# Kernel optimization log

Measured on AMD Instinct MI355X. Metric: run time of the kernel, lower is better.

## Reference

```python
import jax, jax.numpy as jnp
import numpy as np

N = 50000      # node_size
D = 256        # node_F == rel_F (ent_F)
R = 1000       # rel_size
E = 300000     # triple_size == n_edges
DEPTH = 2
KSEL = E // 2  # rows rewritten by W_orth transform
NPROXY = 128


def l2n(x):
    # tf.nn.l2_normalize with eps=1e-12
    return x * jax.lax.rsqrt(jnp.maximum(jnp.sum(x * x, axis=-1, keepdims=True), 1e-12))


def setup_inputs() -> dict:
    key = jax.random.key(0)
    ks = jax.random.split(key, 12)
    features = jax.random.normal(ks[0], (N, D), jnp.float32)
    rel_emb = jax.random.normal(ks[1], (R, D), jnp.float32)
    p = jax.random.normal(ks[2], (N, 1), jnp.float32)            # dynamic_node_kernel
    w_keys = jax.random.normal(ks[3], (DEPTH, D, D), jnp.float32) / np.float32(np.sqrt(D))
    attn_kernels = jax.random.normal(ks[4], (DEPTH, D, 1), jnp.float32) * 0.1
    proxy = jax.random.normal(ks[5], (NPROXY, D * (DEPTH + 1)), jnp.float32) * 0.05
    gate_kernel = jax.random.normal(ks[6], (D * (DEPTH + 1), D * (DEPTH + 1)), jnp.float32) / np.float32(np.sqrt(D * (DEPTH + 1)))
    adj_row = jnp.sort(jax.random.randint(ks[7], (E,), 0, N))    # destination (segment) ids, sorted
    adj_col = jax.random.randint(ks[8], (E,), 0, N)              # neighbor ids
    rel_ids = jax.random.randint(ks[9], (E,), 0, R)              # relation id per triple/edge
    rel_vals = jax.random.uniform(ks[10], (E,), jnp.float32)     # sparse_val per triple
    new_indices = jax.random.randint(ks[11], (KSEL,), 0, E)      # rows updated by w_key
    return dict(features=features, rel_emb=rel_emb, p=p, w_keys=w_keys,
                attn_kernels=attn_kernels, proxy=proxy, gate_kernel=gate_kernel,
                rel_vals=rel_vals, adj_row=adj_row, adj_col=adj_col,
                rel_ids=rel_ids, new_indices=new_indices)


def reference(features, rel_emb, p, w_keys, attn_kernels, proxy, gate_kernel,
              rel_vals, adj_row, adj_col, rel_ids, new_indices):
    tanh_p = jnp.tanh(p)                                   # [N,1]
    feats = features * tanh_p                              # use_p scaling (activation=None -> identity)
    outputs = [feats]
    for l in range(DEPTH):
        # sparse (triple,rel) x rel_emb : one relation per triple -> gather + scale
        rels_sum = rel_vals[:, None] * rel_emb[rel_ids]    # [E,D]
        rels_sum = l2n(rels_sum)
        # W_orth: transform a subset of rows by w_key, scatter back
        src = rels_sum[new_indices] @ w_keys[l]            # [KSEL,D]
        rels_sum = rels_sum.at[new_indices].set(src)
        neighs = feats[adj_col]                            # [E,D] gather
        rels_sum = rels_sum * tanh_p[adj_col]              # use_p on neighbors
        # Householder-style reflection of neighbor features
        neighs = neighs - 2.0 * jnp.sum(neighs * rels_sum, axis=1, keepdims=True) * rels_sum
        # per-edge attention logits, softmax over incoming edges of each row node
        att = (rels_sum @ attn_kernels[l])[:, 0]           # [E]
        m = jax.ops.segment_max(att, adj_row, num_segments=N)      # [N]
        att = jnp.exp(att - m[adj_row])
        s = jax.ops.segment_sum(att, adj_row, num_segments=N)      # [N]
        att = att / s[adj_row]
        # weighted scatter-aggregate
        feats = jax.ops.segment_sum(neighs * att[:, None], adj_row, num_segments=N)  # [N,D]
        feats = feats * tanh_p
        outputs.append(feats)
    out = jnp.concatenate(outputs, axis=-1)                # [N, D*(DEPTH+1)]
    proxy_att = jax.nn.softmax(l2n(out) @ l2n(proxy).T, axis=-1)   # [N,128]
    proxy_feature = out - proxy_att @ proxy
    gate = jax.nn.sigmoid(proxy_feature @ gate_kernel)
    out = gate * out + (1.0 - gate) * proxy_feature
    return (out, p)
```

## Files before the change

kernel.cpp:

```cpp
#include <hip/hip_runtime.h>
#include <math.h>

#define D 256
#define DCAT 768
#define NPX 128
#define QSTR 896
#define CSTR 136

typedef __attribute__((ext_vector_type(8))) short bf16x8;
typedef __attribute__((ext_vector_type(4))) float f32x4;

__device__ __forceinline__ short cvt_bf16(float f){
  union { float f; unsigned u; } v; v.f = f;
  unsigned r = v.u + 0x7FFF + ((v.u >> 16) & 1);
  return (short)(r >> 16);
}
__device__ __forceinline__ float bf2f(short s){
  union { float f; unsigned u; } v; v.u = ((unsigned)(unsigned short)s) << 16;
  return v.f;
}

__device__ __forceinline__ float waveSum(float v){
#pragma unroll
  for(int o=32;o>=1;o>>=1) v += __shfl_xor(v,o,64);
  return v;
}
__device__ __forceinline__ float waveMax(float v){
#pragma unroll
  for(int o=32;o>=1;o>>=1) v = fmaxf(v,__shfl_xor(v,o,64));
  return v;
}

__global__ void k_prep(const float* __restrict__ p, float* __restrict__ tp,
                       const int* __restrict__ adj_row, int* __restrict__ rs,
                       const int* __restrict__ idx, unsigned char* __restrict__ flag,
                       float* __restrict__ pout, int n, int e, int ksel){
  int i = blockIdx.x*blockDim.x+threadIdx.x;
  if(i<n){ float pv = p[i]; tp[i]=tanhf(pv); pout[i]=pv; }
  if(i<=n){
    int lo=0, hi=e;
    while(lo<hi){ int mid=(lo+hi)>>1; if(adj_row[mid]<i) lo=mid+1; else hi=mid; }
    rs[i]=lo;
  }
  if(i<ksel) flag[idx[i]] = 1;
}

__global__ void k_relprep(const float* __restrict__ rel_emb, const float* __restrict__ attn,
                          float* __restrict__ ss_rel, float* __restrict__ att_n,
                          short* __restrict__ reb, int R_){
  __shared__ float sm[4];
  int r = blockIdx.x; int d = threadIdx.x;
  float v = rel_emb[(size_t)r*D+d];
  reb[(size_t)r*D+d] = cvt_bf16(v);
  int lane=threadIdx.x&63, wid=threadIdx.x>>6;
  float s = waveSum(v*v);
  if(lane==0) sm[wid]=s;
  __syncthreads();
  if(threadIdx.x==0) ss_rel[r]=sm[0]+sm[1]+sm[2]+sm[3];
  __syncthreads();
  for(int l=0;l<2;l++){
    float dd = waveSum(v*attn[l*D+d]);
    if(lane==0) sm[wid]=dd;
    __syncthreads();
    if(threadIdx.x==0) att_n[(size_t)l*R_+r]=sm[0]+sm[1]+sm[2]+sm[3];
    __syncthreads();
  }
}

__global__ void k_relW(const float* __restrict__ rel_emb, const float* __restrict__ W,
                       const float* __restrict__ ak, short* __restrict__ rwb,
                       float* __restrict__ att_t, int R_){
  __shared__ float sm[4];
  int r=blockIdx.x, d=threadIdx.x;
  const float* row = rel_emb + (size_t)r*D;
  float acc=0.f;
#pragma unroll 4
  for(int k=0;k<D;k++) acc = fmaf(row[k], W[(size_t)k*D+d], acc);
  rwb[(size_t)r*D+d]=cvt_bf16(acc);
  int lane=threadIdx.x&63, wid=threadIdx.x>>6;
  float dd = waveSum(acc*ak[d]);
  if(lane==0) sm[wid]=dd;
  __syncthreads();
  if(threadIdx.x==0) att_t[r]=sm[0]+sm[1]+sm[2]+sm[3];
}

__global__ void k_init0(const float* __restrict__ features, const float* __restrict__ tp,
                        short* __restrict__ Q, float* __restrict__ ssn, int n){
  __shared__ float sm[4];
  int row = blockIdx.x, d = threadIdx.x;
  float v = features[(size_t)row*D + d] * tp[row];
  Q[(size_t)row*QSTR + d] = cvt_bf16(v);
  int lane=d&63, wid=d>>6;
  float s = waveSum(v*v);
  if(lane==0) sm[wid]=s;
  __syncthreads();
  if(d==0) ssn[row] = sm[0]+sm[1]+sm[2]+sm[3];
}

__global__ void k_agg(const int* __restrict__ rs, const int* __restrict__ adj_col,
                      const int* __restrict__ rel_ids, const float* __restrict__ rel_vals,
                      const unsigned char* __restrict__ flag, const float* __restrict__ tp,
                      const float* __restrict__ ss_rel, const float* __restrict__ att_n,
                      const float* __restrict__ att_t, const short* __restrict__ reb,
                      const short* __restrict__ rwb, short* __restrict__ Q,
                      float* __restrict__ ssn, int n, int layer){
  int wid = threadIdx.x>>6, lane = threadIdx.x&63;
  int node = blockIdx.x*4 + wid;
  if(node>=n) return;
  int s = rs[node], e = rs[node+1];
  float accq[16];
#pragma unroll
  for(int k=0;k<16;k++) accq[k]=0.f;
  if(e > s){
    float mx = -INFINITY;
    for(int i=s+lane;i<e;i+=64){
      int rid = rel_ids[i]; float rv = rel_vals[i];
      float a = 0.f;
      if(rv>0.f){
        float t = tp[adj_col[i]];
        float sc = rv*rsqrtf(fmaxf(rv*rv*ss_rel[rid],1e-12f));
        a = t*sc*(flag[i]? att_t[rid] : att_n[rid]);
      }
      mx = fmaxf(mx,a);
    }
    mx = waveMax(mx);
    float se = 0.f;
    for(int i=s+lane;i<e;i+=64){
      int rid = rel_ids[i]; float rv = rel_vals[i];
      float a = 0.f;
      if(rv>0.f){
        float t = tp[adj_col[i]];
        float sc = rv*rsqrtf(fmaxf(rv*rv*ss_rel[rid],1e-12f));
        a = t*sc*(flag[i]? att_t[rid] : att_n[rid]);
      }
      se += __expf(a-mx);
    }
    se = waveSum(se);
    float inv = 1.f/se;
    int qid = lane>>4, ql = lane&15;
    for(int i0=s; i0<e; i0+=4){
      int j = i0 + qid;
      float w=0.f, coef=0.f;
      float nbv[16], rbv[16];
#pragma unroll
      for(int k=0;k<16;k++){ nbv[k]=0.f; rbv[k]=0.f; }
      if(j < e){
        int rid = rel_ids[j]; float rv = rel_vals[j]; int col = adj_col[j];
        const short* np = Q + (size_t)col*QSTR + layer*D + ql*16;
        bf16x8 n0 = *(const bf16x8*)np;
        bf16x8 n1 = *(const bf16x8*)(np+8);
#pragma unroll
        for(int k=0;k<8;k++){ nbv[k]=bf2f(n0[k]); nbv[k+8]=bf2f(n1[k]); }
        if(rv>0.f){
          float t = tp[col];
          float sc = rv*rsqrtf(fmaxf(rv*rv*ss_rel[rid],1e-12f));
          bool f = flag[j];
          const short* rp = (f? rwb : reb) + (size_t)rid*D + ql*16;
          bf16x8 r0 = *(const bf16x8*)rp;
          bf16x8 r1 = *(const bf16x8*)(rp+8);
#pragma unroll
          for(int k=0;k<8;k++){ rbv[k]=bf2f(r0[k]); rbv[k+8]=bf2f(r1[k]); }
          float dp = 0.f;
#pragma unroll
          for(int k=0;k<16;k++) dp += nbv[k]*rbv[k];
#pragma unroll
          for(int o=1;o<16;o<<=1) dp += __shfl_xor(dp,o,64);
          float a = t*sc*(f? att_t[rid] : att_n[rid]);
          w = __expf(a-mx)*inv;
          coef = 2.f*t*t*sc*sc*dp;
        } else {
          w = __expf(-mx)*inv;
        }
      }
#pragma unroll
      for(int k=0;k<16;k++) accq[k] += w*(nbv[k] - coef*rbv[k]);
    }
  }
#pragma unroll
  for(int k=0;k<16;k++){
    float v = accq[k];
    v += __shfl_xor(v,16,64);
    v += __shfl_xor(v,32,64);
    accq[k] = v;
  }
  if(lane < 16){
    float t0 = tp[node];
    bf16x8 o0, o1;
    float pss = 0.f;
#pragma unroll
    for(int k=0;k<8;k++){
      o0[k]=cvt_bf16(accq[k]*t0); o1[k]=cvt_bf16(accq[k+8]*t0);
      pss += accq[k]*accq[k] + accq[k+8]*accq[k+8];
    }
    short* op = Q + (size_t)node*QSTR + (layer+1)*D + lane*16;
    *(bf16x8*)op = o0;
    *(bf16x8*)(op+8) = o1;
#pragma unroll
    for(int o=1;o<16;o<<=1) pss += __shfl_xor(pss,o,64);
    if(lane==0) ssn[node] += pss * t0 * t0;
  }
}

__global__ void k_proxynorm(const float* __restrict__ proxy, short* __restrict__ pn){
  __shared__ float sm[4];
  int j = blockIdx.x;
  float ssum=0.f;
  for(int d=threadIdx.x; d<DCAT; d+=256){ float v=proxy[(size_t)j*DCAT+d]; ssum+=v*v; }
  int lane=threadIdx.x&63, wid=threadIdx.x>>6;
  ssum = waveSum(ssum);
  if(lane==0) sm[wid]=ssum;
  __syncthreads();
  float scale = rsqrtf(fmaxf(sm[0]+sm[1]+sm[2]+sm[3],1e-12f));
  for(int d=threadIdx.x; d<DCAT; d+=256)
    pn[(size_t)j*DCAT + d] = cvt_bf16(proxy[(size_t)j*DCAT+d]*scale);
}

__global__ void k_cast(const float* __restrict__ in, short* __restrict__ out, long total){
  long i = (long)blockIdx.x*blockDim.x+threadIdx.x;
  if(i<total) out[i]=cvt_bf16(in[i]);
}

__global__ void k_tcast(const float* __restrict__ in, short* __restrict__ out,
                        int R, int C, int ldo, int coff, float sign){
  __shared__ float tile[32][33];
  int bx = blockIdx.x*32, by = blockIdx.y*32;
  for(int i=threadIdx.y;i<32;i+=8){
    int rr = by+i, cc = bx+threadIdx.x;
    if(rr<R && cc<C) tile[i][threadIdx.x] = in[(size_t)rr*C + cc];
  }
  __syncthreads();
  for(int i=threadIdx.y;i<32;i+=8){
    int cc = bx+i, rr = by+threadIdx.x;
    if(cc<C && rr<R) out[(size_t)cc*ldo + coff + rr] = cvt_bf16(sign*tile[threadIdx.x][i]);
  }
}

template<int LDA_, int LDB_, int NTOT, int KC>
__global__ __launch_bounds__(256,2) void k_gemm(
    const short* __restrict__ A, const short* __restrict__ Bt,
    float* __restrict__ outF, int M)
{
  __shared__ short smem[3][2][128*32];
  const int tid = threadIdx.x;
  const int lane = tid & 63, w = tid >> 6;
  const int wm = w >> 1, wn = w & 1;
  const int bn = blockIdx.x * 128, bm = blockIdx.y * 128;

  const short* Ag = A  + (size_t)bm * LDA_;
  const short* Bg = Bt + (size_t)bn * LDB_;

  auto stage = [&](int buf, int k0){
#pragma unroll
    for(int c=0;c<2;++c){
      int u = c*256 + tid;
      int row = u >> 2;
      int cb = ((u & 3) ^ ((u >> 3) & 3)) * 8;
      __builtin_amdgcn_global_load_lds(
        (const __attribute__((address_space(1))) unsigned int*)(Ag + (size_t)row*LDA_ + k0 + cb),
        (__attribute__((address_space(3))) unsigned int*)&smem[buf][0][u*8], 16, 0, 0);
      __builtin_amdgcn_global_load_lds(
        (const __attribute__((address_space(1))) unsigned int*)(Bg + (size_t)row*LDB_ + k0 + cb),
        (__attribute__((address_space(3))) unsigned int*)&smem[buf][1][u*8], 16, 0, 0);
    }
  };

  f32x4 acc[4][4] = {};
  const int lr = lane & 15, kg = lane >> 4;
  const int ksw = (kg ^ ((lr >> 1) & 3)) * 8;
  constexpr int NT = KC / 32;

  stage(0, 0);
  stage(1, 32);
  for(int t=0; t<NT; ++t){
    if(t+1 < NT) asm volatile("s_waitcnt vmcnt(4)" ::: "memory");
    else         asm volatile("s_waitcnt vmcnt(0)" ::: "memory");
    __builtin_amdgcn_s_barrier();
    __builtin_amdgcn_sched_barrier(0);
    const short* Al = &smem[t%3][0][0];
    const short* Bl = &smem[t%3][1][0];
    bf16x8 af[4], bfr[4];
#pragma unroll
    for(int i=0;i<4;++i) af[i] = *(const bf16x8*)(Al + (wm*64 + i*16 + lr)*32 + ksw);
#pragma unroll
    for(int j=0;j<4;++j) bfr[j] = *(const bf16x8*)(Bl + (wn*64 + j*16 + lr)*32 + ksw);
    if(t+2 < NT) stage((t+2)%3, (t+2)*32);
    __builtin_amdgcn_s_setprio(1);
#pragma unroll
    for(int i=0;i<4;++i)
#pragma unroll
      for(int j=0;j<4;++j)
        acc[i][j] = __builtin_amdgcn_mfma_f32_16x16x32_bf16(af[i], bfr[j], acc[i][j], 0, 0, 0);
    __builtin_amdgcn_s_setprio(0);
  }

  const int row0 = bm + wm*64 + (lane>>4)*4;
  const int col0 = bn + wn*64 + lr;
#pragma unroll
  for(int i=0;i<4;++i)
#pragma unroll
    for(int j=0;j<4;++j)
#pragma unroll
      for(int r=0;r<4;++r){
        int row = row0 + i*16 + r;
        if(row < M) outF[(size_t)row*NTOT + col0 + j*16] = acc[i][j][r];
      }
}

__global__ __launch_bounds__(256,2) void k_pr(
    short* __restrict__ Q, const short* __restrict__ pn,
    const float* __restrict__ ssn, int M)
{
  __shared__ short smem[3][2][128*32];
  const int tid = threadIdx.x, lane = tid & 63, w = tid >> 6;
  const int wm = w >> 1, wn = w & 1;
  int nwg = gridDim.y;
  int orig = blockIdx.y;
  int q = nwg>>3, rm = nwg&7, xcd = orig&7, lid = orig>>3;
  int wg = (xcd<rm ? xcd*(q+1) : rm*(q+1)+(xcd-rm)*q) + lid;
  const int bm = wg*128;

  const short* Ag = Q + (size_t)bm * QSTR;
  const short* Bg = pn;

  auto stage = [&](int buf, int k0){
#pragma unroll
    for(int c=0;c<2;++c){
      int u = c*256 + tid;
      int row = u >> 2;
      int cb = ((u & 3) ^ ((u >> 3) & 3)) * 8;
      __builtin_amdgcn_global_load_lds(
        (const __attribute__((address_space(1))) unsigned int*)(Ag + (size_t)row*QSTR + k0 + cb),
        (__attribute__((address_space(3))) unsigned int*)&smem[buf][0][u*8], 16, 0, 0);
      __builtin_amdgcn_global_load_lds(
        (const __attribute__((address_space(1))) unsigned int*)(Bg + (size_t)row*DCAT + k0 + cb),
        (__attribute__((address_space(3))) unsigned int*)&smem[buf][1][u*8], 16, 0, 0);
    }
  };

  f32x4 acc[4][4] = {};
  const int lr = lane & 15, kg = lane >> 4;
  const int ksw = (kg ^ ((lr >> 1) & 3)) * 8;
  constexpr int NT = DCAT / 32;

  stage(0, 0);
  stage(1, 32);
  for(int t=0; t<NT; ++t){
    if(t+1 < NT) asm volatile("s_waitcnt vmcnt(4)" ::: "memory");
    else         asm volatile("s_waitcnt vmcnt(0)" ::: "memory");
    __builtin_amdgcn_s_barrier();
    __builtin_amdgcn_sched_barrier(0);
    const short* Al = &smem[t%3][0][0];
    const short* Bl = &smem[t%3][1][0];
    bf16x8 af[4], bfr[4];
#pragma unroll
    for(int i=0;i<4;++i) af[i] = *(const bf16x8*)(Al + (wm*64 + i*16 + lr)*32 + ksw);
#pragma unroll
    for(int j=0;j<4;++j) bfr[j] = *(const bf16x8*)(Bl + (wn*64 + j*16 + lr)*32 + ksw);
    if(t+2 < NT) stage((t+2)%3, (t+2)*32);
    __builtin_amdgcn_s_setprio(1);
#pragma unroll
    for(int i=0;i<4;++i)
#pragma unroll
      for(int j=0;j<4;++j)
        acc[i][j] = __builtin_amdgcn_mfma_f32_16x16x32_bf16(af[i], bfr[j], acc[i][j], 0, 0, 0);
    __builtin_amdgcn_s_setprio(0);
  }

  __syncthreads();
  short* lg = (short*)smem;
  const int row0l = wm*64 + kg*4;
  const int col0l = wn*64 + lr;
#pragma unroll
  for(int i=0;i<4;++i){
#pragma unroll
    for(int j=0;j<4;++j){
#pragma unroll
      for(int r=0;r<4;++r){
        int rl = row0l + i*16 + r;
        int rg = bm + rl;
        float s = (rg < M) ? rsqrtf(fmaxf(ssn[rg],1e-12f)) : 0.f;
        lg[rl*132 + col0l + j*16] = cvt_bf16(acc[i][j][r] * s);
      }
    }
  }
  __syncthreads();
  for(int k2=0;k2<32;++k2){
    int rl = w*32 + k2;
    float a = bf2f(lg[rl*132 + lane]);
    float b = bf2f(lg[rl*132 + 64 + lane]);
    float m = waveMax(fmaxf(a,b));
    float ea = __expf(a-m), eb = __expf(b-m);
    float sm_ = waveSum(ea+eb);
    float inv = 1.f/sm_;
    size_t rg = (size_t)(bm + rl);
    Q[rg*QSTR + DCAT + lane]      = cvt_bf16(ea*inv);
    Q[rg*QSTR + DCAT + 64 + lane] = cvt_bf16(eb*inv);
  }
}

__global__ __launch_bounds__(256,2) void k_go(
    short* __restrict__ Q, const short* __restrict__ BG,
    const short* __restrict__ Bt2, float* __restrict__ outF, int M)
{
  __shared__ short smem[3][2][128*32];
  const int tid = threadIdx.x, lane = tid & 63, w = tid >> 6;
  const int wm = w >> 1, wn = w & 1;
  const int gx = gridDim.x;
  int nwg = gx*gridDim.y;
  int orig = blockIdx.y*gx + blockIdx.x;
  int q = nwg>>3, rm = nwg&7, xcd = orig&7, lid = orig>>3;
  int wg = (xcd<rm ? xcd*(q+1) : rm*(q+1)+(xcd-rm)*q) + lid;
  const int bn = (wg%gx)*128, bm = (wg/gx)*128;
  const int lr = lane & 15, kg = lane >> 4;

  const short* Ag = Q  + (size_t)bm * QSTR;
  const short* Bg = BG + (size_t)bn * QSTR;

  auto stage = [&](int buf, int k0){
#pragma unroll
    for(int c=0;c<2;++c){
      int u = c*256 + tid;
      int row = u >> 2;
      int cb = ((u & 3) ^ ((u >> 3) & 3)) * 8;
      __builtin_amdgcn_global_load_lds(
        (const __attribute__((address_space(1))) unsigned int*)(Ag + (size_t)row*QSTR + k0 + cb),
        (__attribute__((address_space(3))) unsigned int*)&smem[buf][0][u*8], 16, 0, 0);
      __builtin_amdgcn_global_load_lds(
        (const __attribute__((address_space(1))) unsigned int*)(Bg + (size_t)row*QSTR + k0 + cb),
        (__attribute__((address_space(3))) unsigned int*)&smem[buf][1][u*8], 16, 0, 0);
    }
  };

  stage(0, 0);
  stage(1, 32);

  f32x4 acc[4][4] = {};
#pragma unroll
  for(int ks=0; ks<4; ++ks){
    bf16x8 af[4], bb[4];
#pragma unroll
    for(int i=0;i<4;++i)
      af[i] = *(const bf16x8*)(Q + (size_t)(bm + wm*64 + i*16 + lr)*QSTR + DCAT + ks*32 + kg*8);
#pragma unroll
    for(int j=0;j<4;++j)
      bb[j] = *(const bf16x8*)(Bt2 + (size_t)(bn + wn*64 + j*16 + lr)*NPX + ks*32 + kg*8);
#pragma unroll
    for(int i=0;i<4;++i)
#pragma unroll
      for(int j=0;j<4;++j)
        acc[i][j] = __builtin_amdgcn_mfma_f32_16x16x32_bf16(af[i], bb[j], acc[i][j], 0, 0, 0);
  }
  short4 pvb[4][4];
#pragma unroll
  for(int i=0;i<4;++i)
#pragma unroll
    for(int j=0;j<4;++j){
      pvb[i][j].x = cvt_bf16(acc[i][j][0]);
      pvb[i][j].y = cvt_bf16(acc[i][j][1]);
      pvb[i][j].z = cvt_bf16(acc[i][j][2]);
      pvb[i][j].w = cvt_bf16(acc[i][j][3]);
      acc[i][j] = (f32x4){0.f,0.f,0.f,0.f};
    }

  const int ksw = (kg ^ ((lr >> 1) & 3)) * 8;
  constexpr int NT = QSTR / 32;
  for(int t=0; t<NT; ++t){
    if(t+1 < NT) asm volatile("s_waitcnt vmcnt(4)" ::: "memory");
    else         asm volatile("s_waitcnt vmcnt(0)" ::: "memory");
    __builtin_amdgcn_s_barrier();
    __builtin_amdgcn_sched_barrier(0);
    const short* Al = &smem[t%3][0][0];
    const short* Bl = &smem[t%3][1][0];
    bf16x8 af[4], bfr[4];
#pragma unroll
    for(int i=0;i<4;++i) af[i] = *(const bf16x8*)(Al + (wm*64 + i*16 + lr)*32 + ksw);
#pragma unroll
    for(int j=0;j<4;++j) bfr[j] = *(const bf16x8*)(Bl + (wn*64 + j*16 + lr)*32 + ksw);
    if(t+2 < NT) stage((t+2)%3, (t+2)*32);
    __builtin_amdgcn_s_setprio(1);
#pragma unroll
    for(int i=0;i<4;++i)
#pragma unroll
      for(int j=0;j<4;++j)
        acc[i][j] = __builtin_amdgcn_mfma_f32_16x16x32_bf16(af[i], bfr[j], acc[i][j], 0, 0, 0);
    __builtin_amdgcn_s_setprio(0);
  }

  __syncthreads();
  short* cst = (short*)smem;
  const int row0l = wm*64 + kg*4;
  const int col0l = wn*64 + lr;
#pragma unroll
  for(int i=0;i<4;++i){
#pragma unroll
    for(int j=0;j<4;++j){
      float pv4[4] = { bf2f(pvb[i][j].x), bf2f(pvb[i][j].y), bf2f(pvb[i][j].z), bf2f(pvb[i][j].w) };
#pragma unroll
      for(int r2=0;r2<4;++r2){
        float g = 1.f/(1.f+__expf(-acc[i][j][r2]));
        cst[(row0l + i*16 + r2)*CSTR + col0l + j*16] = cvt_bf16((1.f-g)*pv4[r2]);
      }
    }
  }
  __syncthreads();
  const int rl0 = tid>>4, c0 = (tid&15)*8;
#pragma unroll
  for(int rr=0; rr<8; ++rr){
    int rl = rl0 + rr*16;
    int rg = bm + rl;
    if(rg >= M) continue;
    bf16x8 c8  = *(const bf16x8*)(cst + rl*CSTR + c0);
    bf16x8 oc8 = *(const bf16x8*)(Q + (size_t)rg*QSTR + bn + c0);
    float ov[8];
#pragma unroll
    for(int k=0;k<8;k++) ov[k] = bf2f(oc8[k]) - bf2f(c8[k]);
    *(float4*)(outF + (size_t)rg*DCAT + bn + c0)     = make_float4(ov[0],ov[1],ov[2],ov[3]);
    *(float4*)(outF + (size_t)rg*DCAT + bn + c0 + 4) = make_float4(ov[4],ov[5],ov[6],ov[7]);
  }
}

extern "C" void kernel_launch(void* const* d_in, const int* in_sizes, int n_in,
                              void* d_out, int out_size, void* d_ws, size_t ws_size,
                              hipStream_t stream){
  const float* features = (const float*)d_in[0];
  const float* rel_emb  = (const float*)d_in[1];
  const float* p        = (const float*)d_in[2];
  const float* w_keys   = (const float*)d_in[3];
  const float* attn     = (const float*)d_in[4];
  const float* proxy    = (const float*)d_in[5];
  const float* gatek    = (const float*)d_in[6];
  const float* rel_vals = (const float*)d_in[7];
  const int* adj_row    = (const int*)d_in[8];
  const int* adj_col    = (const int*)d_in[9];
  const int* rel_ids    = (const int*)d_in[10];
  const int* new_idx    = (const int*)d_in[11];

  const int n    = in_sizes[2];
  const int r    = in_sizes[1]/D;
  const int e    = in_sizes[7];
  const int ksel = in_sizes[11];
  const size_t Mpad = ((size_t)n + 127) & ~(size_t)127;

  char* ws = (char*)d_ws;
  size_t off=0;
  auto alloc=[&](size_t bytes)->void*{ void* pp = ws+off; off=(off+bytes+255)&~(size_t)255; return pp; };
  float* tp      = (float*)alloc((size_t)n*4);
  int*   rs      = (int*)alloc((size_t)(n+1)*4);
  unsigned char* flag = (unsigned char*)alloc((size_t)e);
  float* ss_rel  = (float*)alloc((size_t)r*4);
  float* att_n   = (float*)alloc((size_t)2*r*4);
  float* att_t   = (float*)alloc((size_t)2*r*4);
  short* reb     = (short*)alloc((size_t)r*D*2);
  short* rwb     = (short*)alloc((size_t)2*r*D*2);
  short* pn      = (short*)alloc((size_t)NPX*DCAT*2);
  short* proxyb  = (short*)alloc((size_t)NPX*DCAT*2);
  short* Bt2     = (short*)alloc((size_t)DCAT*NPX*2);
  short* BG      = (short*)alloc((size_t)DCAT*QSTR*2);
  float* MxF     = (float*)alloc((size_t)NPX*DCAT*4);
  float* ssn     = (float*)alloc(Mpad*4);
  short* Q       = (short*)alloc(Mpad*QSTR*2);

  float* outF = (float*)d_out;
  float* pout = (float*)d_out + (size_t)n*DCAT;

  hipMemsetAsync(flag, 0, (size_t)e, stream);
  hipMemsetAsync(Q + (size_t)n*QSTR, 0, (Mpad-(size_t)n)*QSTR*2, stream);

  int prep_n = (ksel > n+1 ? ksel : n+1);
  k_prep<<<(prep_n+255)/256,256,0,stream>>>(p,tp,adj_row,rs,new_idx,flag,pout,n,e,ksel);
  k_relprep<<<r,256,0,stream>>>(rel_emb,attn,ss_rel,att_n,reb,r);
  for(int l=0;l<2;l++)
    k_relW<<<r,256,0,stream>>>(rel_emb, w_keys+(size_t)l*D*D, attn+(size_t)l*D,
                               rwb+(size_t)l*r*D, att_t+(size_t)l*r, r);
  k_proxynorm<<<NPX,256,0,stream>>>(proxy,pn);
  {
    long tpx = (long)NPX*DCAT;
    k_cast<<<(int)((tpx+255)/256),256,0,stream>>>(proxy, proxyb, tpx);
    dim3 tb(32,8);
    k_tcast<<<dim3(DCAT/32, DCAT/32), tb, 0, stream>>>(gatek, BG, DCAT, DCAT, QSTR, 0, 1.f);
    k_gemm<DCAT, QSTR, DCAT, DCAT><<<dim3(DCAT/128,1),256,0,stream>>>(proxyb, BG, MxF, NPX);
    k_tcast<<<dim3(DCAT/32, NPX/32), tb, 0, stream>>>(MxF, BG, NPX, DCAT, QSTR, DCAT, -1.f);
    k_tcast<<<dim3(DCAT/32, NPX/32), tb, 0, stream>>>(proxy, Bt2, NPX, DCAT, NPX, 0, 1.f);
  }
  k_init0<<<n,256,0,stream>>>(features,tp,Q,ssn,n);
  for(int l=0;l<2;l++)
    k_agg<<<(n+3)/4,256,0,stream>>>(rs,adj_col,rel_ids,rel_vals,flag,tp,ss_rel,
                                    att_n+(size_t)l*r, att_t+(size_t)l*r, reb,
                                    rwb+(size_t)l*r*D, Q, ssn, n, l);

  int mt = (int)(Mpad/128);
  k_pr<<<dim3(1, mt),256,0,stream>>>(Q, pn, ssn, n);
  k_go<<<dim3(DCAT/128, mt),256,0,stream>>>(Q, BG, Bt2, outF, n);
}
```

Measured before the change: 495.9 us.

## Enlarge k_go row tile to 256 with 512 threads and defer proxy GEMM

The gate GEMM kernel now uses 512-thread workgroups that compute 256-row by 128-column tiles. Each B tile staged in LDS is therefore reused by eight waves instead of four, which cuts B-side global traffic per output. The small proxy_att@proxy GEMM is moved from before the main K loop to after it, so its bf16 results no longer occupy registers during the pipelined loop. In exchange the launch has half as many workgroups, uses more LDS per block, and pads M to 256, which can lower occupancy and load balance.

After: 505.5 us. About the same (+1.9%).

```diff
diff --git a/kernel.cpp b/kernel.cpp
--- a/kernel.cpp
+++ b/kernel.cpp
@@ -398,20 +398,20 @@
   }
 }
 
-__global__ __launch_bounds__(256,2) void k_go(
+__global__ __launch_bounds__(512,2) void k_go(
     short* __restrict__ Q, const short* __restrict__ BG,
     const short* __restrict__ Bt2, float* __restrict__ outF, int M)
 {
-  __shared__ short smem[3][2][128*32];
+  __shared__ short smem[3][384*32];
   const int tid = threadIdx.x, lane = tid & 63, w = tid >> 6;
   const int wm = w >> 1, wn = w & 1;
+  const int lr = lane & 15, kg = lane >> 4;
   const int gx = gridDim.x;
   int nwg = gx*gridDim.y;
   int orig = blockIdx.y*gx + blockIdx.x;
   int q = nwg>>3, rm = nwg&7, xcd = orig&7, lid = orig>>3;
   int wg = (xcd<rm ? xcd*(q+1) : rm*(q+1)+(xcd-rm)*q) + lid;
-  const int bn = (wg%gx)*128, bm = (wg/gx)*128;
-  const int lr = lane & 15, kg = lane >> 4;
+  const int bn = (wg%gx)*128, bm = (wg/gx)*256;
 
   const short* Ag = Q  + (size_t)bm * QSTR;
   const short* Bg = BG + (size_t)bn * QSTR;
@@ -419,15 +419,20 @@
   auto stage = [&](int buf, int k0){
 #pragma unroll
     for(int c=0;c<2;++c){
-      int u = c*256 + tid;
+      int u = c*512 + tid;
       int row = u >> 2;
       int cb = ((u & 3) ^ ((u >> 3) & 3)) * 8;
       __builtin_amdgcn_global_load_lds(
         (const __attribute__((address_space(1))) unsigned int*)(Ag + (size_t)row*QSTR + k0 + cb),
-        (__attribute__((address_space(3))) unsigned int*)&smem[buf][0][u*8], 16, 0, 0);
+        (__attribute__((address_space(3))) unsigned int*)&smem[buf][u*8], 16, 0, 0);
+    }
+    {
+      int u = tid;
+      int row = u >> 2;
+      int cb = ((u & 3) ^ ((u >> 3) & 3)) * 8;
       __builtin_amdgcn_global_load_lds(
         (const __attribute__((address_space(1))) unsigned int*)(Bg + (size_t)row*QSTR + k0 + cb),
-        (__attribute__((address_space(3))) unsigned int*)&smem[buf][1][u*8], 16, 0, 0);
+        (__attribute__((address_space(3))) unsigned int*)&smem[buf][8192 + u*8], 16, 0, 0);
     }
   };
 
@@ -435,42 +440,15 @@
   stage(1, 32);
 
   f32x4 acc[4][4] = {};
-#pragma unroll
-  for(int ks=0; ks<4; ++ks){
-    bf16x8 af[4], bb[4];
-#pragma unroll
-    for(int i=0;i<4;++i)
-      af[i] = *(const bf16x8*)(Q + (size_t)(bm + wm*64 + i*16 + lr)*QSTR + DCAT + ks*32 + kg*8);
-#pragma unroll
-    for(int j=0;j<4;++j)
-      bb[j] = *(const bf16x8*)(Bt2 + (size_t)(bn + wn*64 + j*16 + lr)*NPX + ks*32 + kg*8);
-#pragma unroll
-    for(int i=0;i<4;++i)
-#pragma unroll
-      for(int j=0;j<4;++j)
-        acc[i][j] = __builtin_amdgcn_mfma_f32_16x16x32_bf16(af[i], bb[j], acc[i][j], 0, 0, 0);
-  }
-  short4 pvb[4][4];
-#pragma unroll
-  for(int i=0;i<4;++i)
-#pragma unroll
-    for(int j=0;j<4;++j){
-      pvb[i][j].x = cvt_bf16(acc[i][j][0]);
-      pvb[i][j].y = cvt_bf16(acc[i][j][1]);
-      pvb[i][j].z = cvt_bf16(acc[i][j][2]);
-      pvb[i][j].w = cvt_bf16(acc[i][j][3]);
-      acc[i][j] = (f32x4){0.f,0.f,0.f,0.f};
-    }
-
   const int ksw = (kg ^ ((lr >> 1) & 3)) * 8;
   constexpr int NT = QSTR / 32;
   for(int t=0; t<NT; ++t){
-    if(t+1 < NT) asm volatile("s_waitcnt vmcnt(4)" ::: "memory");
+    if(t+1 < NT) asm volatile("s_waitcnt vmcnt(3)" ::: "memory");
     else         asm volatile("s_waitcnt vmcnt(0)" ::: "memory");
     __builtin_amdgcn_s_barrier();
     __builtin_amdgcn_sched_barrier(0);
-    const short* Al = &smem[t%3][0][0];
-    const short* Bl = &smem[t%3][1][0];
+    const short* Al = &smem[t%3][0];
+    const short* Bl = &smem[t%3][0] + 8192;
     bf16x8 af[4], bfr[4];
 #pragma unroll
     for(int i=0;i<4;++i) af[i] = *(const bf16x8*)(Al + (wm*64 + i*16 + lr)*32 + ksw);
@@ -486,27 +464,51 @@
     __builtin_amdgcn_s_setprio(0);
   }
 
+  short4 omg[4][4];
+#pragma unroll
+  for(int i=0;i<4;++i)
+#pragma unroll
+    for(int j=0;j<4;++j){
+      omg[i][j].x = cvt_bf16(1.f - 1.f/(1.f+__expf(-acc[i][j][0])));
+      omg[i][j].y = cvt_bf16(1.f - 1.f/(1.f+__expf(-acc[i][j][1])));
+      omg[i][j].z = cvt_bf16(1.f - 1.f/(1.f+__expf(-acc[i][j][2])));
+      omg[i][j].w = cvt_bf16(1.f - 1.f/(1.f+__expf(-acc[i][j][3])));
+    }
+
+  f32x4 pv[4][4] = {};
+#pragma unroll
+  for(int ks=0; ks<4; ++ks){
+    bf16x8 af2[4];
+#pragma unroll
+    for(int i=0;i<4;++i)
+      af2[i] = *(const bf16x8*)(Q + (size_t)(bm + wm*64 + i*16 + lr)*QSTR + DCAT + ks*32 + kg*8);
+#pragma unroll
+    for(int j=0;j<4;++j){
+      bf16x8 bb = *(const bf16x8*)(Bt2 + (size_t)(bn + wn*64 + j*16 + lr)*NPX + ks*32 + kg*8);
+#pragma unroll
+      for(int i=0;i<4;++i)
+        pv[i][j] = __builtin_amdgcn_mfma_f32_16x16x32_bf16(af2[i], bb, pv[i][j], 0, 0, 0);
+    }
+  }
+
   __syncthreads();
   short* cst = (short*)smem;
   const int row0l = wm*64 + kg*4;
   const int col0l = wn*64 + lr;
 #pragma unroll
-  for(int i=0;i<4;++i){
+  for(int i=0;i<4;++i)
 #pragma unroll
     for(int j=0;j<4;++j){
-      float pv4[4] = { bf2f(pvb[i][j].x), bf2f(pvb[i][j].y), bf2f(pvb[i][j].z), bf2f(pvb[i][j].w) };
-#pragma unroll
-      for(int r2=0;r2<4;++r2){
-        float g = 1.f/(1.f+__expf(-acc[i][j][r2]));
-        cst[(row0l + i*16 + r2)*CSTR + col0l + j*16] = cvt_bf16((1.f-g)*pv4[r2]);
-      }
-    }
-  }
+      float o4[4] = { bf2f(omg[i][j].x), bf2f(omg[i][j].y), bf2f(omg[i][j].z), bf2f(omg[i][j].w) };
+#pragma unroll
+      for(int r2=0;r2<4;++r2)
+        cst[(row0l + i*16 + r2)*CSTR + col0l + j*16] = cvt_bf16(o4[r2]*pv[i][j][r2]);
+    }
   __syncthreads();
   const int rl0 = tid>>4, c0 = (tid&15)*8;
 #pragma unroll
   for(int rr=0; rr<8; ++rr){
-    int rl = rl0 + rr*16;
+    int rl = rl0 + rr*32;
     int rg = bm + rl;
     if(rg >= M) continue;
     bf16x8 c8  = *(const bf16x8*)(cst + rl*CSTR + c0);
@@ -539,7 +541,7 @@
   const int r    = in_sizes[1]/D;
   const int e    = in_sizes[7];
   const int ksel = in_sizes[11];
-  const size_t Mpad = ((size_t)n + 127) & ~(size_t)127;
+  const size_t Mpad = ((size_t)n + 255) & ~(size_t)255;
 
   char* ws = (char*)d_ws;
   size_t off=0;
@@ -588,7 +590,6 @@
                                     att_n+(size_t)l*r, att_t+(size_t)l*r, reb,
                                     rwb+(size_t)l*r*D, Q, ssn, n, l);
 
-  int mt = (int)(Mpad/128);
-  k_pr<<<dim3(1, mt),256,0,stream>>>(Q, pn, ssn, n);
-  k_go<<<dim3(DCAT/128, mt),256,0,stream>>>(Q, BG, Bt2, outF, n);
-}
+  k_pr<<<dim3(1, (int)(Mpad/128)),256,0,stream>>>(Q, pn, ssn, n);
+  k_go<<<dim3(DCAT/128, (int)(Mpad/256)),512,0,stream>>>(Q, BG, Bt2, outF, n);
+}
```

## Fuse setup kernels into one launch and prefetch edge metadata in aggregation

Applied to the files above, without the earlier changes.

Merges the relation prep, the two relation-weight projections, the proxy normalisation and cast, and the gate and proxy transposes into a single multi-role k_setup kernel. This cuts launch count and lets these independent jobs run concurrently. In k_agg, the first logit per lane is cached so the exp-sum pass recomputes one fewer logit. The next edge's column, relation id, value and flag are also loaded one iteration ahead to hide gather latency. The costs are higher register use in k_agg and block-role branching in k_setup.

New measurement: 444.3 us. 1.12x faster.

```diff
diff --git a/kernel.cpp b/kernel.cpp
--- a/kernel.cpp
+++ b/kernel.cpp
@@ -45,43 +45,94 @@
   if(i<ksel) flag[idx[i]] = 1;
 }
 
-__global__ void k_relprep(const float* __restrict__ rel_emb, const float* __restrict__ attn,
-                          float* __restrict__ ss_rel, float* __restrict__ att_n,
-                          short* __restrict__ reb, int R_){
+__global__ void k_setup(const float* __restrict__ rel_emb, const float* __restrict__ attn,
+                        const float* __restrict__ w_keys, const float* __restrict__ proxy,
+                        const float* __restrict__ gatek,
+                        float* __restrict__ ss_rel, float* __restrict__ att_n,
+                        float* __restrict__ att_t, short* __restrict__ reb,
+                        short* __restrict__ rwb, short* __restrict__ pn,
+                        short* __restrict__ proxyb, short* __restrict__ BG,
+                        short* __restrict__ Bt2, int R_){
+  __shared__ float tile[32][33];
   __shared__ float sm[4];
-  int r = blockIdx.x; int d = threadIdx.x;
-  float v = rel_emb[(size_t)r*D+d];
-  reb[(size_t)r*D+d] = cvt_bf16(v);
-  int lane=threadIdx.x&63, wid=threadIdx.x>>6;
-  float s = waveSum(v*v);
-  if(lane==0) sm[wid]=s;
+  const int b = blockIdx.x, tid = threadIdx.x;
+  const int lane = tid & 63, wv = tid >> 6;
+
+  if(b < R_){
+    int r = b, d = tid;
+    float v = rel_emb[(size_t)r*D+d];
+    reb[(size_t)r*D+d] = cvt_bf16(v);
+    float s = waveSum(v*v);
+    if(lane==0) sm[wv]=s;
+    __syncthreads();
+    if(tid==0) ss_rel[r]=sm[0]+sm[1]+sm[2]+sm[3];
+    __syncthreads();
+    for(int l=0;l<2;l++){
+      float dd = waveSum(v*attn[l*D+d]);
+      if(lane==0) sm[wv]=dd;
+      __syncthreads();
+      if(tid==0) att_n[(size_t)l*R_+r]=sm[0]+sm[1]+sm[2]+sm[3];
+      __syncthreads();
+    }
+  } else if(b < 3*R_){
+    int l = (b-R_) / R_, r = (b-R_) % R_, d = tid;
+    const float* W = w_keys + (size_t)l*D*D;
+    const float* ak = attn + (size_t)l*D;
+    const float* row = rel_emb + (size_t)r*D;
+    float acc=0.f;
+#pragma unroll 4
+    for(int k=0;k<D;k++) acc = fmaf(row[k], W[(size_t)k*D+d], acc);
+    rwb[(size_t)l*R_*D + (size_t)r*D + d]=cvt_bf16(acc);
+    float dd = waveSum(acc*ak[d]);
+    if(lane==0) sm[wv]=dd;
+    __syncthreads();
+    if(tid==0) att_t[(size_t)l*R_+r]=sm[0]+sm[1]+sm[2]+sm[3];
+  } else if(b < 3*R_+128){
+    int j = b - 3*R_;
+    float v0 = proxy[(size_t)j*DCAT + tid];
+    float v1 = proxy[(size_t)j*DCAT + 256 + tid];
+    float v2 = proxy[(size_t)j*DCAT + 512 + tid];
+    proxyb[(size_t)j*DCAT + tid]       = cvt_bf16(v0);
+    proxyb[(size_t)j*DCAT + 256 + tid] = cvt_bf16(v1);
+    proxyb[(size_t)j*DCAT + 512 + tid] = cvt_bf16(v2);
+    float ssum = waveSum(v0*v0 + v1*v1 + v2*v2);
+    if(lane==0) sm[wv]=ssum;
+    __syncthreads();
+    float scale = rsqrtf(fmaxf(sm[0]+sm[1]+sm[2]+sm[3],1e-12f));
+    pn[(size_t)j*DCAT + tid]       = cvt_bf16(v0*scale);
+    pn[(size_t)j*DCAT + 256 + tid] = cvt_bf16(v1*scale);
+    pn[(size_t)j*DCAT + 512 + tid] = cvt_bf16(v2*scale);
+  } else {
+    const float* in; short* out; int R, C, ldo, coff, t;
+    if(b < 3*R_+128+576){ t = b-(3*R_+128);     in=gatek; out=BG;  R=DCAT; C=DCAT; ldo=QSTR; coff=0; }
+    else                { t = b-(3*R_+128+576); in=proxy; out=Bt2; R=NPX;  C=DCAT; ldo=NPX;  coff=0; }
+    int bx = (t%24)*32, by = (t/24)*32;
+    int tx = tid & 31, ty = tid >> 5;
+    for(int i=ty;i<32;i+=8){
+      int rr = by+i, cc = bx+tx;
+      if(rr<R && cc<C) tile[i][tx] = in[(size_t)rr*C + cc];
+    }
+    __syncthreads();
+    for(int i=ty;i<32;i+=8){
+      int cc = bx+i, rr = by+tx;
+      if(cc<C && rr<R) out[(size_t)cc*ldo + coff + rr] = cvt_bf16(tile[tx][i]);
+    }
+  }
+}
+
+__global__ void k_tcast(const float* __restrict__ in, short* __restrict__ out,
+                        int R, int C, int ldo, int coff, float sign){
+  __shared__ float tile[32][33];
+  int bx = blockIdx.x*32, by = blockIdx.y*32;
+  for(int i=threadIdx.y;i<32;i+=8){
+    int rr = by+i, cc = bx+threadIdx.x;
+    if(rr<R && cc<C) tile[i][threadIdx.x] = in[(size_t)rr*C + cc];
+  }
   __syncthreads();
-  if(threadIdx.x==0) ss_rel[r]=sm[0]+sm[1]+sm[2]+sm[3];
-  __syncthreads();
-  for(int l=0;l<2;l++){
-    float dd = waveSum(v*attn[l*D+d]);
-    if(lane==0) sm[wid]=dd;
-    __syncthreads();
-    if(threadIdx.x==0) att_n[(size_t)l*R_+r]=sm[0]+sm[1]+sm[2]+sm[3];
-    __syncthreads();
-  }
-}
-
-__global__ void k_relW(const float* __restrict__ rel_emb, const float* __restrict__ W,
-                       const float* __restrict__ ak, short* __restrict__ rwb,
-                       float* __restrict__ att_t, int R_){
-  __shared__ float sm[4];
-  int r=blockIdx.x, d=threadIdx.x;
-  const float* row = rel_emb + (size_t)r*D;
-  float acc=0.f;
-#pragma unroll 4
-  for(int k=0;k<D;k++) acc = fmaf(row[k], W[(size_t)k*D+d], acc);
-  rwb[(size_t)r*D+d]=cvt_bf16(acc);
-  int lane=threadIdx.x&63, wid=threadIdx.x>>6;
-  float dd = waveSum(acc*ak[d]);
-  if(lane==0) sm[wid]=dd;
-  __syncthreads();
-  if(threadIdx.x==0) att_t[r]=sm[0]+sm[1]+sm[2]+sm[3];
+  for(int i=threadIdx.y;i<32;i+=8){
+    int cc = bx+i, rr = by+threadIdx.x;
+    if(cc<C && rr<R) out[(size_t)cc*ldo + coff + rr] = cvt_bf16(sign*tile[threadIdx.x][i]);
+  }
 }
 
 __global__ void k_init0(const float* __restrict__ features, const float* __restrict__ tp,
@@ -111,41 +162,50 @@
   float accq[16];
 #pragma unroll
   for(int k=0;k<16;k++) accq[k]=0.f;
+
+  auto logit = [&](int i)->float{
+    int rid = rel_ids[i]; float rv = rel_vals[i];
+    float a = 0.f;
+    if(rv>0.f){
+      float t = tp[adj_col[i]];
+      float sc = rv*rsqrtf(fmaxf(rv*rv*ss_rel[rid],1e-12f));
+      a = t*sc*(flag[i]? att_t[rid] : att_n[rid]);
+    }
+    return a;
+  };
+
   if(e > s){
-    float mx = -INFINITY;
-    for(int i=s+lane;i<e;i+=64){
-      int rid = rel_ids[i]; float rv = rel_vals[i];
-      float a = 0.f;
-      if(rv>0.f){
-        float t = tp[adj_col[i]];
-        float sc = rv*rsqrtf(fmaxf(rv*rv*ss_rel[rid],1e-12f));
-        a = t*sc*(flag[i]? att_t[rid] : att_n[rid]);
+    float aF = 0.f, mxl = -INFINITY;
+    {
+      int i = s + lane;
+      if(i < e){
+        aF = logit(i);
+        mxl = aF;
+        for(i += 64; i < e; i += 64) mxl = fmaxf(mxl, logit(i));
       }
-      mx = fmaxf(mx,a);
-    }
-    mx = waveMax(mx);
-    float se = 0.f;
-    for(int i=s+lane;i<e;i+=64){
-      int rid = rel_ids[i]; float rv = rel_vals[i];
-      float a = 0.f;
-      if(rv>0.f){
-        float t = tp[adj_col[i]];
-        float sc = rv*rsqrtf(fmaxf(rv*rv*ss_rel[rid],1e-12f));
-        a = t*sc*(flag[i]? att_t[rid] : att_n[rid]);
-      }
-      se += __expf(a-mx);
-    }
-    se = waveSum(se);
+    }
+    float mx = waveMax(mxl);
+    float sel = (s+lane < e) ? __expf(aF - mx) : 0.f;
+    for(int i = s+64+lane; i < e; i += 64) sel += __expf(logit(i) - mx);
+    float se = waveSum(sel);
     float inv = 1.f/se;
+
     int qid = lane>>4, ql = lane&15;
+    int j0 = s + qid;
+    bool valid = j0 < e;
+    int col=0, rid=0; float rv=0.f; bool fl=false;
+    if(valid){ col=adj_col[j0]; rid=rel_ids[j0]; rv=rel_vals[j0]; fl=flag[j0]; }
     for(int i0=s; i0<e; i0+=4){
-      int j = i0 + qid;
+      int jn = i0 + 4 + qid;
+      bool vn = jn < e;
+      int coln=0, ridn=0; float rvn=0.f; bool fln=false;
+      if(vn){ coln=adj_col[jn]; ridn=rel_ids[jn]; rvn=rel_vals[jn]; fln=flag[jn]; }
+
       float w=0.f, coef=0.f;
       float nbv[16], rbv[16];
 #pragma unroll
       for(int k=0;k<16;k++){ nbv[k]=0.f; rbv[k]=0.f; }
-      if(j < e){
-        int rid = rel_ids[j]; float rv = rel_vals[j]; int col = adj_col[j];
+      if(valid){
         const short* np = Q + (size_t)col*QSTR + layer*D + ql*16;
         bf16x8 n0 = *(const bf16x8*)np;
         bf16x8 n1 = *(const bf16x8*)(np+8);
@@ -154,8 +214,7 @@
         if(rv>0.f){
           float t = tp[col];
           float sc = rv*rsqrtf(fmaxf(rv*rv*ss_rel[rid],1e-12f));
-          bool f = flag[j];
-          const short* rp = (f? rwb : reb) + (size_t)rid*D + ql*16;
+          const short* rp = (fl? rwb : reb) + (size_t)rid*D + ql*16;
           bf16x8 r0 = *(const bf16x8*)rp;
           bf16x8 r1 = *(const bf16x8*)(rp+8);
 #pragma unroll
@@ -165,7 +224,7 @@
           for(int k=0;k<16;k++) dp += nbv[k]*rbv[k];
 #pragma unroll
           for(int o=1;o<16;o<<=1) dp += __shfl_xor(dp,o,64);
-          float a = t*sc*(f? att_t[rid] : att_n[rid]);
+          float a = t*sc*(fl? att_t[rid] : att_n[rid]);
           w = __expf(a-mx)*inv;
           coef = 2.f*t*t*sc*sc*dp;
         } else {
@@ -174,6 +233,8 @@
       }
 #pragma unroll
       for(int k=0;k<16;k++) accq[k] += w*(nbv[k] - coef*rbv[k]);
+
+      valid=vn; col=coln; rid=ridn; rv=rvn; fl=fln;
     }
   }
 #pragma unroll
@@ -198,40 +259,6 @@
 #pragma unroll
     for(int o=1;o<16;o<<=1) pss += __shfl_xor(pss,o,64);
     if(lane==0) ssn[node] += pss * t0 * t0;
-  }
-}
-
-__global__ void k_proxynorm(const float* __restrict__ proxy, short* __restrict__ pn){
-  __shared__ float sm[4];
-  int j = blockIdx.x;
-  float ssum=0.f;
-  for(int d=threadIdx.x; d<DCAT; d+=256){ float v=proxy[(size_t)j*DCAT+d]; ssum+=v*v; }
-  int lane=threadIdx.x&63, wid=threadIdx.x>>6;
-  ssum = waveSum(ssum);
-  if(lane==0) sm[wid]=ssum;
-  __syncthreads();
-  float scale = rsqrtf(fmaxf(sm[0]+sm[1]+sm[2]+sm[3],1e-12f));
-  for(int d=threadIdx.x; d<DCAT; d+=256)
-    pn[(size_t)j*DCAT + d] = cvt_bf16(proxy[(size_t)j*DCAT+d]*scale);
-}
-
-__global__ void k_cast(const float* __restrict__ in, short* __restrict__ out, long total){
-  long i = (long)blockIdx.x*blockDim.x+threadIdx.x;
-  if(i<total) out[i]=cvt_bf16(in[i]);
-}
-
-__global__ void k_tcast(const float* __restrict__ in, short* __restrict__ out,
-                        int R, int C, int ldo, int coff, float sign){
-  __shared__ float tile[32][33];
-  int bx = blockIdx.x*32, by = blockIdx.y*32;
-  for(int i=threadIdx.y;i<32;i+=8){
-    int rr = by+i, cc = bx+threadIdx.x;
-    if(rr<R && cc<C) tile[i][threadIdx.x] = in[(size_t)rr*C + cc];
-  }
-  __syncthreads();
-  for(int i=threadIdx.y;i<32;i+=8){
-    int cc = bx+i, rr = by+threadIdx.x;
-    if(cc<C && rr<R) out[(size_t)cc*ldo + coff + rr] = cvt_bf16(sign*tile[threadIdx.x][i]);
   }
 }
 
@@ -568,20 +595,15 @@
 
   int prep_n = (ksel > n+1 ? ksel : n+1);
   k_prep<<<(prep_n+255)/256,256,0,stream>>>(p,tp,adj_row,rs,new_idx,flag,pout,n,e,ksel);
-  k_relprep<<<r,256,0,stream>>>(rel_emb,attn,ss_rel,att_n,reb,r);
-  for(int l=0;l<2;l++)
-    k_relW<<<r,256,0,stream>>>(rel_emb, w_keys+(size_t)l*D*D, attn+(size_t)l*D,
-                               rwb+(size_t)l*r*D, att_t+(size_t)l*r, r);
-  k_proxynorm<<<NPX,256,0,stream>>>(proxy,pn);
   {
-    long tpx = (long)NPX*DCAT;
-    k_cast<<<(int)((tpx+255)/256),256,0,stream>>>(proxy, proxyb, tpx);
-    dim3 tb(32,8);
-    k_tcast<<<dim3(DCAT/32, DCAT/32), tb, 0, stream>>>(gatek, BG, DCAT, DCAT, QSTR, 0, 1.f);
-    k_gemm<DCAT, QSTR, DCAT, DCAT><<<dim3(DCAT/128,1),256,0,stream>>>(proxyb, BG, MxF, NPX);
-    k_tcast<<<dim3(DCAT/32, NPX/32), tb, 0, stream>>>(MxF, BG, NPX, DCAT, QSTR, DCAT, -1.f);
-    k_tcast<<<dim3(DCAT/32, NPX/32), tb, 0, stream>>>(proxy, Bt2, NPX, DCAT, NPX, 0, 1.f);
-  }
+    int nblocks = 3*r + 128 + 576 + 96;
+    k_setup<<<nblocks,256,0,stream>>>(rel_emb, attn, w_keys, proxy, gatek,
+                                      ss_rel, att_n, att_t, reb, rwb, pn, proxyb,
+                                      BG, Bt2, r);
+  }
+  k_gemm<DCAT, QSTR, DCAT, DCAT><<<dim3(DCAT/128,1),256,0,stream>>>(proxyb, BG, MxF, NPX);
+  k_tcast<<<dim3(DCAT/32, NPX/32), dim3(32,8), 0, stream>>>(MxF, BG, NPX, DCAT, QSTR, DCAT, -1.f);
+
   k_init0<<<n,256,0,stream>>>(features,tp,Q,ssn,n);
   for(int l=0;l<2;l++)
     k_agg<<<(n+3)/4,256,0,stream>>>(rs,adj_col,rel_ids,rel_vals,flag,tp,ss_rel,
```
